# Optimization experiments

Measured on AMD Instinct MI355X. Metric: run time of the kernel, lower is better.

## Reference

```python
import jax, jax.numpy as jnp
import numpy as np

DECAY = 0.999
EPS = 1e-5
COMMIT = 0.25
ORTHO_W = 10.0
NUM_ORTHO = 128


def setup_inputs() -> dict:
    key = jax.random.key(0)
    k1, k2 = jax.random.split(key)
    M, D = 2048, 512
    B, T = 32, 1024
    x = jax.random.normal(k1, (B, T, D), dtype=jnp.float32)
    init_bound = 1.0 / M
    emb = jax.random.uniform(k2, (M, D), minval=-init_bound, maxval=init_bound, dtype=jnp.float32)
    return {
        "x": x,
        "embedding": emb,
        "ema_count": jnp.zeros((M,), jnp.float32),
        "ema_weight": emb,  # torch init: ema_weight = embedding.clone()
    }


def reference(x, embedding, ema_count, ema_weight):
    M, D = embedding.shape
    x_sg = jax.lax.stop_gradient(x)
    x_flat = x_sg.reshape(-1, D)  # [N, D]

    distances = (jnp.sum(embedding * embedding, axis=1)[None, :]
                 + jnp.sum(x_flat * x_flat, axis=1, keepdims=True)
                 - 2.0 * (x_flat @ embedding.T))
    indices = jnp.argmin(distances.astype(jnp.float32), axis=-1)  # [N]

    quantized = embedding[indices].reshape(x.shape)

    # EMA updates (training=True). one_hot(indices).sum(0) == scatter-add counts;
    # encodings.T @ x_flat == scatter-add of x rows into code slots.
    counts = jnp.zeros((M,), x.dtype).at[indices].add(1.0)
    new_count = DECAY * ema_count + (1.0 - DECAY) * counts
    n = jnp.sum(new_count)
    new_count = (new_count + EPS) / (n + M * EPS) * n
    dw = jnp.zeros((M, D), x.dtype).at[indices].add(x_flat)
    new_weight = DECAY * ema_weight + (1.0 - DECAY) * dw
    new_embedding = new_weight / new_count[:, None]

    codebook_loss = jnp.mean((x_sg - quantized) ** 2)
    e_latent_loss = jnp.mean((x - jax.lax.stop_gradient(quantized)) ** 2)
    commitment_loss = COMMIT * e_latent_loss

    quant_st = x + jax.lax.stop_gradient(quantized - x)  # straight-through

    # ortho loss over used codes of the UPDATED codebook (torch: self.embedding post-EMA).
    # Deterministic jit-safe variant of unique+randperm: take the first NUM_ORTHO
    # used code ids (stable argsort puts used codes first), mask padding if fewer.
    used = counts > 0
    order = jnp.argsort(jnp.where(used, 0, 1).astype(jnp.int32))  # stable sort
    sel = order[:NUM_ORTHO]
    valid = used[sel].astype(x.dtype)  # [NUM_ORTHO]
    codebk = new_embedding[sel]
    norm = jnp.maximum(jnp.linalg.norm(codebk, axis=-1, keepdims=True), 1e-12)
    normed = (codebk / norm) * valid[:, None]
    cosine_sim = normed @ normed.T
    n_valid = jnp.sum(valid)
    ortho_loss = jnp.sum((cosine_sim - jnp.diag(valid)) ** 2) / (n_valid * n_valid) * ORTHO_W

    return (quant_st, commitment_loss, codebook_loss, ortho_loss, indices,
            new_embedding, new_count, new_weight)
```

## Files before the change

### kernel.cpp

```cpp
#include <hip/hip_runtime.h>
#include <math.h>

#define N_ROWS 32768
#define M_CODES 2048
#define D_DIM 512
#define MARGIN 1.2e-3f
#define CAND_CAP 32

#define OUT_QST       0
#define OUT_COMMIT    16777216
#define OUT_CODEBOOK  16777217
#define OUT_ORTHO     16777218
#define OUT_INDICES   16777219
#define OUT_NEWEMB    16809987
#define OUT_NEWCOUNT  17858563
#define OUT_NEWW      17860611

#define WS_COUNTS     0
#define WS_CURSOR     2048
#define WS_SSE        4096
#define WS_ORTHO      4097
#define WS_CANDCNT    4104
#define WS_ZERO_FLOATS 36872
#define WS_E2         36872
#define WS_X2         38920
#define WS_IDX        71688
#define WS_NCN        104456
#define WS_SEL        106504
#define WS_VALID      106632
#define WS_NVALID     106760
#define WS_NORMED     106768
#define WS_NORMEDT    172304
#define WS_OFFS       237840
#define WS_ORDER      239896
#define WS_CANDC      272664
#define WS_CANDD      1321240
#define WS_XH         2369816
#define WS_EH         10758424
#define WS_TOTAL_FLOATS 11282712

typedef __attribute__((ext_vector_type(8))) short short8v;
typedef __attribute__((ext_vector_type(4))) float f32x4;

__device__ __forceinline__ unsigned short f2bf(float f) {
    unsigned u = __float_as_uint(f);
    unsigned r = (u + 0x7fffu + ((u >> 16) & 1u)) >> 16;
    return (unsigned short)r;
}
__device__ __forceinline__ int fkey(float f) {
    int b = __float_as_int(f);
    return b >= 0 ? b : (b ^ 0x7fffffff);
}
__device__ __forceinline__ float kinv(int k) {
    int b = k >= 0 ? k : (k ^ 0x7fffffff);
    return __int_as_float(b);
}

#define GLOAD16(g, s) __builtin_amdgcn_global_load_lds( \
    (const __attribute__((address_space(1))) void*)(g), \
    (__attribute__((address_space(3))) void*)(s), 16, 0, 0)

__global__ __launch_bounds__(256) void prep_kernel(const float* __restrict__ emb,
                                                   const float* __restrict__ x,
                                                   float* __restrict__ e2,
                                                   float* __restrict__ x2,
                                                   unsigned short* __restrict__ xh,
                                                   unsigned short* __restrict__ eh) {
    int row  = blockIdx.x * 4 + (threadIdx.x >> 6);
    int lane = threadIdx.x & 63;
    bool is_e = row < M_CODES;
    const float* src = is_e ? (emb + (size_t)row * D_DIM)
                            : (x + (size_t)(row - M_CODES) * D_DIM);
    unsigned short* dh = is_e ? (eh + (size_t)row * D_DIM)
                              : (xh + (size_t)(row - M_CODES) * D_DIM);
    float4 a = *(const float4*)(src + lane * 4);
    float4 b = *(const float4*)(src + 256 + lane * 4);
    float s = a.x*a.x + a.y*a.y + a.z*a.z + a.w*a.w
            + b.x*b.x + b.y*b.y + b.z*b.z + b.w*b.w;
#pragma unroll
    for (int o = 32; o > 0; o >>= 1) s += __shfl_xor(s, o, 64);

    ushort4 h0, h1;
    h0.x = f2bf(a.x); h0.y = f2bf(a.y); h0.z = f2bf(a.z); h0.w = f2bf(a.w);
    h1.x = f2bf(b.x); h1.y = f2bf(b.y); h1.z = f2bf(b.z); h1.w = f2bf(b.w);
    *(ushort4*)(dh + lane * 4)       = h0;
    *(ushort4*)(dh + 256 + lane * 4) = h1;

    if (lane == 0) {
        if (is_e) e2[row] = s;
        else      x2[row - M_CODES] = s;
    }
}

__global__ __launch_bounds__(256) void sq_kernel(const float* __restrict__ emb,
                                                 const float* __restrict__ x,
                                                 float* __restrict__ e2,
                                                 float* __restrict__ x2) {
    int row  = blockIdx.x * 4 + (threadIdx.x >> 6);
    int lane = threadIdx.x & 63;
    const float* src = (row < M_CODES) ? (emb + (size_t)row * D_DIM)
                                       : (x + (size_t)(row - M_CODES) * D_DIM);
    float4 a = *(const float4*)(src + lane * 4);
    float4 b = *(const float4*)(src + 256 + lane * 4);
    float s = a.x*a.x + a.y*a.y + a.z*a.z + a.w*a.w
            + b.x*b.x + b.y*b.y + b.z*b.z + b.w*b.w;
#pragma unroll
    for (int o = 32; o > 0; o >>= 1) s += __shfl_xor(s, o, 64);
    if (lane == 0) {
        if (row < M_CODES) e2[row] = s;
        else               x2[row - M_CODES] = s;
    }
}

__global__ __launch_bounds__(256) void approx_kernel(const unsigned short* __restrict__ xh,
                                                     const unsigned short* __restrict__ eh,
                                                     const float* __restrict__ e2g,
                                                     int* __restrict__ candcnt,
                                                     int* __restrict__ candC,
                                                     float* __restrict__ candD) {
    __shared__ short Ah[128 * 64], Bh[128 * 64];
    __shared__ int rowminI[128];

    const int t = threadIdx.x;
    const int w = t >> 6;
    const int l = t & 63;
    const int ml = l & 15;
    const int q  = l >> 4;
    const int rw = (w & 1) * 64;
    const int cw = (w >> 1) * 64;

    const int bid = blockIdx.x;
    const int row_tile = (bid >> 5) * 8 + (bid & 7);
    const int sub = (bid >> 3) & 3;
    const int row0 = row_tile * 128;
    const int code_base = sub * 512;

    if (t < 128) rowminI[t] = 0x7fffffff;

    const int grow = l >> 3;
    const int pg8  = (((l & 7) ^ grow)) * 8;

    for (int ct = 0; ct < 4; ++ct) {
        const int code0 = code_base + ct * 128;

        f32x4 acc[4][4];
#pragma unroll
        for (int mi = 0; mi < 4; ++mi)
#pragma unroll
            for (int ni = 0; ni < 4; ++ni) acc[mi][ni] = (f32x4)0.f;

        for (int k0 = 0; k0 < D_DIM; k0 += 64) {
            __syncthreads();
#pragma unroll
            for (int i = 0; i < 4; ++i) {
                int r = i * 32 + w * 8 + grow;
                GLOAD16(xh + (size_t)(row0 + r) * D_DIM + k0 + pg8, &Ah[i * 2048 + w * 512]);
                GLOAD16(eh + (size_t)(code0 + r) * D_DIM + k0 + pg8, &Bh[i * 2048 + w * 512]);
            }
            __syncthreads();

#pragma unroll
            for (int kk = 0; kk < 64; kk += 32) {
                const int pbase = kk >> 3;
                short8v a[4];
#pragma unroll
                for (int mi = 0; mi < 4; ++mi) {
                    int m = rw + mi * 16 + ml;
                    a[mi] = *(const short8v*)(&Ah[m * 64 + ((((pbase + q) ^ (m & 7))) << 3)]);
                }
#pragma unroll
                for (int ni = 0; ni < 4; ++ni) {
                    int n = cw + ni * 16 + ml;
                    short8v b = *(const short8v*)(&Bh[n * 64 + ((((pbase + q) ^ (n & 7))) << 3)]);
#pragma unroll
                    for (int mi = 0; mi < 4; ++mi)
                        acc[mi][ni] = __builtin_amdgcn_mfma_f32_16x16x32_bf16(a[mi], b, acc[mi][ni], 0, 0, 0);
                }
            }
        }

        float e2v[4];
#pragma unroll
        for (int ni = 0; ni < 4; ++ni) e2v[ni] = e2g[code0 + cw + ni * 16 + ml];

#pragma unroll
        for (int mi = 0; mi < 4; ++mi)
#pragma unroll
            for (int ni = 0; ni < 4; ++ni)
#pragma unroll
                for (int r = 0; r < 4; ++r)
                    acc[mi][ni][r] = e2v[ni] - 2.0f * acc[mi][ni][r];

#pragma unroll
        for (int mi = 0; mi < 4; ++mi)
#pragma unroll
            for (int r = 0; r < 4; ++r) {
                float v = fminf(fminf(acc[mi][0][r], acc[mi][1][r]),
                                fminf(acc[mi][2][r], acc[mi][3][r]));
#pragma unroll
                for (int o = 1; o < 16; o <<= 1) v = fminf(v, __shfl_xor(v, o, 64));
                if (ml == 0) atomicMin(&rowminI[rw + mi * 16 + q * 4 + r], fkey(v));
            }
        __syncthreads();

#pragma unroll
        for (int mi = 0; mi < 4; ++mi)
#pragma unroll
            for (int r = 0; r < 4; ++r) {
                int row_l = rw + mi * 16 + q * 4 + r;
                float rm = kinv(rowminI[row_l]);
                int row_g = row0 + row_l;
#pragma unroll
                for (int ni = 0; ni < 4; ++ni) {
                    float d = acc[mi][ni][r];
                    if (d <= rm + MARGIN) {
                        int pos = atomicAdd(&candcnt[row_g], 1);
                        if (pos < CAND_CAP) {
                            candC[row_g * CAND_CAP + pos] = code0 + cw + ni * 16 + ml;
                            candD[row_g * CAND_CAP + pos] = d;
                        }
                    }
                }
            }
    }
}

__global__ __launch_bounds__(256) void rerank_kernel(const float* __restrict__ x,
                                                     const float* __restrict__ emb,
                                                     const float* __restrict__ e2,
                                                     const float* __restrict__ x2,
                                                     const int* __restrict__ candcnt,
                                                     const int* __restrict__ candC,
                                                     const float* __restrict__ candD,
                                                     float* __restrict__ counts,
                                                     int* __restrict__ idx_out,
                                                     float* __restrict__ idxf_out) {
    const int w = threadIdx.x >> 6;
    const int lane = threadIdx.x & 63;
    const int row = blockIdx.x * 4 + w;

    int cnt = candcnt[row];
    int best_c;

    if (cnt > CAND_CAP) {
        const float x2r = x2[row];
        const float* xr = x + (size_t)row * D_DIM;
        float bd = 3.0e38f;
        int   bc = 0x7fffffff;
        for (int c = lane; c < M_CODES; c += 64) {
            const float* er = emb + (size_t)c * D_DIM;
            float dot = 0.f;
            for (int k = 0; k < D_DIM; ++k) dot = fmaf(xr[k], er[k], dot);
            float d = (x2r + e2[c]) - 2.0f * dot;
            if (d < bd || (d == bd && c < bc)) { bd = d; bc = c; }
        }
#pragma unroll
        for (int o = 32; o > 0; o >>= 1) {
            float od = __shfl_xor(bd, o, 64);
            int   oc = __shfl_xor(bc, o, 64);
            if (od < bd || (od == bd && oc < bc)) { bd = od; bc = oc; }
        }
        best_c = bc;
    } else {
        float d = 3.0e38f;
        int   c = 0x7fffffff;
        if (lane < cnt) {
            d = candD[row * CAND_CAP + lane];
            c = candC[row * CAND_CAP + lane];
        }
        float dmin = d;
#pragma unroll
        for (int o = 32; o > 0; o >>= 1) dmin = fminf(dmin, __shfl_xor(dmin, o, 64));

        bool surv = (lane < cnt) && (d <= dmin + MARGIN);
        unsigned long long mask = __ballot(surv);

        if (__popcll(mask) == 1) {
            int src = __ffsll((long long)mask) - 1;
            best_c = __shfl(c, src, 64);
        } else {
            const float x2r = x2[row];
            const float* xr = x + (size_t)row * D_DIM;
            float4 xa = *(const float4*)(xr + lane * 8);
            float4 xb = *(const float4*)(xr + lane * 8 + 4);
            float bd = 3.0e38f;
            int   bc = 0x7fffffff;
            unsigned long long m = mask;
            while (m) {
                int src = __ffsll((long long)m) - 1;
                m &= m - 1;
                int cs = __shfl(c, src, 64);
                const float* er = emb + (size_t)cs * D_DIM;
                float4 ea = *(const float4*)(er + lane * 8);
                float4 eb = *(const float4*)(er + lane * 8 + 4);
                float dot = xa.x*ea.x + xa.y*ea.y + xa.z*ea.z + xa.w*ea.w
                          + xb.x*eb.x + xb.y*eb.y + xb.z*eb.z + xb.w*eb.w;
#pragma unroll
                for (int o = 32; o > 0; o >>= 1) dot += __shfl_xor(dot, o, 64);
                float t1 = x2r + e2[cs];
                float dex = t1 - 2.0f * dot;
                if (dex < bd || (dex == bd && cs < bc)) { bd = dex; bc = cs; }
            }
            best_c = bc;
        }
    }
    if (lane == 0) {
        idx_out[row] = best_c;
        idxf_out[row] = (float)best_c;
        atomicAdd(&counts[best_c], 1.0f);
    }
}

__global__ __launch_bounds__(256) void argmin_kernel(const float* __restrict__ x,
                                                     const float* __restrict__ emb,
                                                     const float* __restrict__ e2,
                                                     const float* __restrict__ x2,
                                                     int* __restrict__ idx_out,
                                                     float* __restrict__ idxf_out) {
    __shared__ float As[64][36];
    __shared__ float Bs[32][68];
    __shared__ float e2s[64];
    __shared__ float redD[64][17];
    __shared__ int   redI[64][17];

    const int t  = threadIdx.x;
    const int tx = t & 15;
    const int ty = t >> 4;
    const int row0 = blockIdx.x * 64;

    float rmin[4];
    int   ridx[4];
#pragma unroll
    for (int r = 0; r < 4; ++r) { rmin[r] = 3.0e38f; ridx[r] = 0; }

    float x2r[4];
#pragma unroll
    for (int r = 0; r < 4; ++r) x2r[r] = x2[row0 + ty * 4 + r];

    const int lr = t >> 3;
    const int lc = t & 7;

    for (int m0 = 0; m0 < M_CODES; m0 += 64) {
        __syncthreads();
        if (t < 64) e2s[t] = e2[m0 + t];

        float acc[4][4];
#pragma unroll
        for (int r = 0; r < 4; ++r)
#pragma unroll
            for (int c = 0; c < 4; ++c) acc[r][c] = 0.f;

        for (int k0 = 0; k0 < D_DIM; k0 += 32) {
            __syncthreads();
#pragma unroll
            for (int p = 0; p < 2; ++p) {
                int r = p * 32 + lr;
                float4 v = *(const float4*)(x + (size_t)(row0 + r) * D_DIM + k0 + lc * 4);
                *(float4*)(&As[r][lc * 4]) = v;
            }
#pragma unroll
            for (int p = 0; p < 2; ++p) {
                int r = p * 32 + lr;
                float4 v = *(const float4*)(emb + (size_t)(m0 + r) * D_DIM + k0 + lc * 4);
                Bs[lc * 4 + 0][r] = v.x;
                Bs[lc * 4 + 1][r] = v.y;
                Bs[lc * 4 + 2][r] = v.z;
                Bs[lc * 4 + 3][r] = v.w;
            }
            __syncthreads();

#pragma unroll
            for (int kk = 0; kk < 32; kk += 4) {
                float av[4][4], bv[4][4];
#pragma unroll
                for (int r = 0; r < 4; ++r) {
                    float4 a4 = *(const float4*)(&As[ty * 4 + r][kk]);
                    av[r][0] = a4.x; av[r][1] = a4.y; av[r][2] = a4.z; av[r][3] = a4.w;
                }
#pragma unroll
                for (int j = 0; j < 4; ++j) {
                    float4 b4 = *(const float4*)(&Bs[kk + j][tx * 4]);
                    bv[j][0] = b4.x; bv[j][1] = b4.y; bv[j][2] = b4.z; bv[j][3] = b4.w;
                }
#pragma unroll
                for (int j = 0; j < 4; ++j)
#pragma unroll
                    for (int r = 0; r < 4; ++r)
#pragma unroll
                        for (int c = 0; c < 4; ++c)
                            acc[r][c] += av[r][j] * bv[j][c];
            }
        }

#pragma unroll
        for (int c = 0; c < 4; ++c) {
            int mm = tx * 4 + c;
            int m  = m0 + mm;
            float e2v = e2s[mm];
#pragma unroll
            for (int r = 0; r < 4; ++r) {
                float t1 = x2r[r] + e2v;
                float dd  = t1 - 2.0f * acc[r][c];
                if (dd < rmin[r]) { rmin[r] = dd; ridx[r] = m; }
            }
        }
    }

    __syncthreads();
#pragma unroll
    for (int r = 0; r < 4; ++r) {
        redD[ty * 4 + r][tx] = rmin[r];
        redI[ty * 4 + r][tx] = ridx[r];
    }
    __syncthreads();
    if (t < 64) {
        float best = redD[t][0];
        int   bi   = redI[t][0];
#pragma unroll
        for (int i = 1; i < 16; ++i) {
            float dd = redD[t][i];
            int   ii = redI[t][i];
            if (dd < best || (dd == best && ii < bi)) { best = dd; bi = ii; }
        }
        idx_out[row0 + t]  = bi;
        idxf_out[row0 + t] = (float)bi;
    }
}

__global__ __launch_bounds__(256) void hist_kernel(const int* __restrict__ idx,
                                                   float* __restrict__ counts) {
    int r = blockIdx.x * 256 + threadIdx.x;
    atomicAdd(&counts[idx[r]], 1.0f);
}

__global__ __launch_bounds__(256) void qst_sse_kernel(const float* __restrict__ x,
                                                      const float* __restrict__ emb,
                                                      const int* __restrict__ idx,
                                                      float* __restrict__ sse,
                                                      float* __restrict__ qst) {
    const int w    = threadIdx.x >> 6;
    const int lane = threadIdx.x & 63;
    const int rowbase = blockIdx.x * 16 + w * 4;
    float loss = 0.f;
    for (int i = 0; i < 4; ++i) {
        const int row = rowbase + i;
        const int m   = idx[row];
#pragma unroll
        for (int j = 0; j < 2; ++j) {
            const int off = j * 256 + lane * 4;
            float4 xv = *(const float4*)(x + (size_t)row * D_DIM + off);
            float4 qv = *(const float4*)(emb + (size_t)m * D_DIM + off);
            float4 qs;
            qs.x = xv.x + (qv.x - xv.x);
            qs.y = xv.y + (qv.y - xv.y);
            qs.z = xv.z + (qv.z - xv.z);
            qs.w = xv.w + (qv.w - xv.w);
            *(float4*)(qst + (size_t)row * D_DIM + off) = qs;
            float dx;
            dx = xv.x - qv.x; loss += dx * dx;
            dx = xv.y - qv.y; loss += dx * dx;
            dx = xv.z - qv.z; loss += dx * dx;
            dx = xv.w - qv.w; loss += dx * dx;
        }
    }
#pragma unroll
    for (int o = 32; o > 0; o >>= 1) loss += __shfl_xor(loss, o, 64);
    if (lane == 0) atomicAdd(sse, loss);
}

__global__ __launch_bounds__(256) void f1_kernel(const float* __restrict__ ema_count,
                                                 const float* __restrict__ counts,
                                                 float* __restrict__ out_newcount,
                                                 float* __restrict__ nc_ws) {
    __shared__ float red[256];
    int t = threadIdx.x;
    float raw[8];
    float part = 0.f;
#pragma unroll
    for (int i = 0; i < 8; ++i) {
        int m = t * 8 + i;
        raw[i] = 0.999f * ema_count[m] + 0.001f * counts[m];
        part += raw[i];
    }
    red[t] = part;
    __syncthreads();
    for (int s = 128; s > 0; s >>= 1) {
        if (t < s) red[t] += red[t + s];
        __syncthreads();
    }
    float n = red[0];
    float denom = n + (float)M_CODES * 1e-5f;
#pragma unroll
    for (int i = 0; i < 8; ++i) {
        int m = t * 8 + i;
        float v = (raw[i] + 1e-5f) / denom * n;
        out_newcount[m] = v;
        nc_ws[m] = v;
    }
}

__global__ __launch_bounds__(256) void scan_kernel(const float* __restrict__ counts,
                                                   int* __restrict__ offs) {
    __shared__ int pre[257];
    int t = threadIdx.x;
    int c[8];
    int s = 0;
#pragma unroll
    for (int i = 0; i < 8; ++i) { c[i] = (int)counts[t * 8 + i]; s += c[i]; }
    pre[t] = s;
    __syncthreads();
    if (t == 0) {
        int run = 0;
        for (int i = 0; i < 256; ++i) { int v = pre[i]; pre[i] = run; run += v; }
        pre[256] = run;
    }
    __syncthreads();
    int base = pre[t];
#pragma unroll
    for (int i = 0; i < 8; ++i) { offs[t * 8 + i] = base; base += c[i]; }
}

__global__ __launch_bounds__(256) void fill_kernel(const int* __restrict__ idx,
                                                   const int* __restrict__ offs,
                                                   int* __restrict__ cursor,
                                                   int* __restrict__ order) {
    int r = blockIdx.x * 256 + threadIdx.x;
    int m = idx[r];
    int pos = atomicAdd(&cursor[m], 1);
    order[offs[m] + pos] = r;
}

__global__ __launch_bounds__(256) void gather_nw_kernel(const float* __restrict__ x,
                                                        const float* __restrict__ ema_weight,
                                                        const float* __restrict__ ncn,
                                                        const float* __restrict__ counts,
                                                        const int* __restrict__ offs,
                                                        const int* __restrict__ order,
                                                        float* __restrict__ out_ne,
                                                        float* __restrict__ out_nw) {
    const int m = blockIdx.x;
    const int t = threadIdx.x;
    const int beg = offs[m];
    const int end = beg + (int)counts[m];
    float ax = 0.f, ay = 0.f;
    for (int j = beg; j < end; ++j) {
        int r = order[j];
        float2 v = *(const float2*)(x + (size_t)r * D_DIM + t * 2);
        ax += v.x; ay += v.y;
    }
    size_t i = (size_t)m * D_DIM + t * 2;
    float2 wv = *(const float2*)(ema_weight + i);
    float  c  = ncn[m];
    float2 nw, ne;
    nw.x = 0.999f * wv.x + 0.001f * ax; ne.x = nw.x / c;
    nw.y = 0.999f * wv.y + 0.001f * ay; ne.y = nw.y / c;
    *(float2*)(out_nw + i) = nw;
    *(float2*)(out_ne + i) = ne;
}

__global__ __launch_bounds__(256) void g1_kernel(const float* __restrict__ counts,
                                                 const float* __restrict__ new_emb,
                                                 int* __restrict__ sel,
                                                 float* __restrict__ valid,
                                                 float* __restrict__ n_valid,
                                                 float* __restrict__ normed,
                                                 float* __restrict__ normedT) {
    __shared__ int pre[257];
    int t = threadIdx.x;
    int u = 0;
#pragma unroll
    for (int i = 0; i < 8; ++i) u += (counts[t * 8 + i] > 0.f) ? 1 : 0;
    pre[t] = u;
    __syncthreads();
    if (t == 0) {
        int run = 0;
        for (int i = 0; i < 256; ++i) { int c = pre[i]; pre[i] = run; run += c; }
        pre[256] = run;
    }
    __syncthreads();
    int U = pre[256];
    int base = pre[t];
    int run = 0;
    for (int i = 0; i < 8; ++i) {
        int m = t * 8 + i;
        bool used = counts[m] > 0.f;
        int ur = base + run;
        if (used) {
            if (ur < 128) sel[ur] = m;
            run++;
        } else {
            int pos = U + (m - ur);
            if (pos < 128) sel[pos] = m;
        }
    }
    __syncthreads();
    if (t < 128) valid[t] = (counts[sel[t]] > 0.f) ? 1.f : 0.f;
    __syncthreads();
    if (t == 0) {
        float s = 0.f;
        for (int i = 0; i < 128; ++i) s += valid[i];
        *n_valid = s;
    }
    int w = t >> 6, lane = t & 63;
    for (int r = w; r < 128; r += 4) {
        int sm = sel[r];
        const float* src = new_emb + (size_t)sm * D_DIM;
        float4 a = *(const float4*)(src + lane * 4);
        float4 b = *(const float4*)(src + 256 + lane * 4);
        float s = a.x*a.x + a.y*a.y + a.z*a.z + a.w*a.w
                + b.x*b.x + b.y*b.y + b.z*b.z + b.w*b.w;
#pragma unroll
        for (int o = 32; o > 0; o >>= 1) s += __shfl_xor(s, o, 64);
        float norm = fmaxf(sqrtf(s), 1e-12f);
        float vv = valid[r];
        float4 na, nb;
        na.x = a.x / norm * vv; na.y = a.y / norm * vv;
        na.z = a.z / norm * vv; na.w = a.w / norm * vv;
        nb.x = b.x / norm * vv; nb.y = b.y / norm * vv;
        nb.z = b.z / norm * vv; nb.w = b.w / norm * vv;
        *(float4*)(normed + (size_t)r * D_DIM + lane * 4) = na;
        *(float4*)(normed + (size_t)r * D_DIM + 256 + lane * 4) = nb;
        normedT[(lane * 4 + 0) * 128 + r] = na.x;
        normedT[(lane * 4 + 1) * 128 + r] = na.y;
        normedT[(lane * 4 + 2) * 128 + r] = na.z;
        normedT[(lane * 4 + 3) * 128 + r] = na.w;
        normedT[(256 + lane * 4 + 0) * 128 + r] = nb.x;
        normedT[(256 + lane * 4 + 1) * 128 + r] = nb.y;
        normedT[(256 + lane * 4 + 2) * 128 + r] = nb.z;
        normedT[(256 + lane * 4 + 3) * 128 + r] = nb.w;
    }
}

__global__ __launch_bounds__(128) void g2_kernel(const float* __restrict__ normed,
                                                 const float* __restrict__ normedT,
                                                 const float* __restrict__ valid,
                                                 float* __restrict__ ortho_acc) {
    __shared__ float rowi[512];
    __shared__ float red[128];
    int i = blockIdx.x, t = threadIdx.x;
    *(float4*)(rowi + t * 4) = *(const float4*)(normed + (size_t)i * D_DIM + t * 4);
    __syncthreads();
    float dot = 0.f;
    for (int k = 0; k < D_DIM; ++k) dot += rowi[k] * normedT[k * 128 + t];
    float diag = (i == t) ? valid[i] : 0.f;
    float d = dot - diag;
    red[t] = d * d;
    __syncthreads();
    for (int s = 64; s > 0; s >>= 1) {
        if (t < s) red[t] += red[t + s];
        __syncthreads();
    }
    if (t == 0) atomicAdd(ortho_acc, red[0]);
}

__global__ void g3_kernel(const float* __restrict__ sse,
                          const float* __restrict__ ortho_acc,
                          const float* __restrict__ n_valid,
                          float* __restrict__ out3) {
    if (threadIdx.x == 0 && blockIdx.x == 0) {
        float m = *sse / 16777216.f;
        out3[0] = 0.25f * m;
        out3[1] = m;
        float nv = *n_valid;
        out3[2] = *ortho_acc / (nv * nv) * 10.f;
    }
}

extern "C" void kernel_launch(void* const* d_in, const int* in_sizes, int n_in,
                              void* d_out, int out_size, void* d_ws, size_t ws_size,
                              hipStream_t stream) {
    const float* x          = (const float*)d_in[0];
    const float* emb        = (const float*)d_in[1];
    const float* ema_count  = (const float*)d_in[2];
    const float* ema_weight = (const float*)d_in[3];
    float* out = (float*)d_out;
    float* ws  = (float*)d_ws;

    float* counts  = ws + WS_COUNTS;
    int*   cursor  = (int*)(ws + WS_CURSOR);
    float* sse     = ws + WS_SSE;
    float* ortho   = ws + WS_ORTHO;
    int*   candcnt = (int*)(ws + WS_CANDCNT);
    float* e2      = ws + WS_E2;
    float* x2      = ws + WS_X2;
    int*   idxws   = (int*)(ws + WS_IDX);
    float* ncn     = ws + WS_NCN;
    int*   sel     = (int*)(ws + WS_SEL);
    float* valid   = ws + WS_VALID;
    float* nvalid  = ws + WS_NVALID;
    float* normed  = ws + WS_NORMED;
    float* normedT = ws + WS_NORMEDT;
    int*   offs    = (int*)(ws + WS_OFFS);
    int*   order   = (int*)(ws + WS_ORDER);
    int*   candC   = (int*)(ws + WS_CANDC);
    float* candD   = ws + WS_CANDD;
    unsigned short* xh = (unsigned short*)(ws + WS_XH);
    unsigned short* eh = (unsigned short*)(ws + WS_EH);

    const bool big_ws = ws_size >= (size_t)WS_TOTAL_FLOATS * sizeof(float);

    hipMemsetAsync(ws, 0, (size_t)WS_ZERO_FLOATS * sizeof(float), stream);

    if (big_ws) {
        prep_kernel<<<(M_CODES + N_ROWS) / 4, 256, 0, stream>>>(emb, x, e2, x2, xh, eh);
        approx_kernel<<<1024, 256, 0, stream>>>(xh, eh, e2, candcnt, candC, candD);
        rerank_kernel<<<N_ROWS / 4, 256, 0, stream>>>(x, emb, e2, x2, candcnt, candC, candD,
                                                      counts, idxws, out + OUT_INDICES);
    } else {
        sq_kernel<<<(M_CODES + N_ROWS) / 4, 256, 0, stream>>>(emb, x, e2, x2);
        argmin_kernel<<<N_ROWS / 64, 256, 0, stream>>>(x, emb, e2, x2, idxws,
                                                       out + OUT_INDICES);
        hist_kernel<<<N_ROWS / 256, 256, 0, stream>>>(idxws, counts);
    }

    qst_sse_kernel<<<N_ROWS / 16, 256, 0, stream>>>(x, emb, idxws, sse, out + OUT_QST);

    f1_kernel<<<1, 256, 0, stream>>>(ema_count, counts, out + OUT_NEWCOUNT, ncn);

    scan_kernel<<<1, 256, 0, stream>>>(counts, offs);

    fill_kernel<<<N_ROWS / 256, 256, 0, stream>>>(idxws, offs, cursor, order);

    gather_nw_kernel<<<M_CODES, 256, 0, stream>>>(x, ema_weight, ncn, counts, offs, order,
                                                  out + OUT_NEWEMB, out + OUT_NEWW);

    g1_kernel<<<1, 256, 0, stream>>>(counts, out + OUT_NEWEMB, sel, valid, nvalid,
                                     normed, normedT);

    g2_kernel<<<128, 128, 0, stream>>>(normed, normedT, valid, ortho);

    g3_kernel<<<1, 64, 0, stream>>>(sse, ortho, nvalid, out + OUT_COMMIT);
}
```

Measured before the change: 559.3 us.

## Rewrite approximate distance GEMM with register-resident X fragments and direct global B loads

Replaces the LDS-tiled bf16 MFMA approximate-distance kernel with one where each wave keeps its 32 rows of X for the full 512-wide K in registers and streams codebook fragments straight from global memory (relying on cache) in 64-code chunks. Each block now covers 1024 codes instead of 512, and the running row minimum is held in registers per wave instead of a shared atomicMin, so the LDS staging and block-wide syncs go away. Because the candidate threshold now uses a running minimum, more candidates may be emitted early in the scan, which raises atomic traffic and the risk of overflowing the candidate cap. Holding 32 short8 vectors of X per lane also adds heavy register pressure.

```diff
diff --git a/kernel.cpp b/kernel.cpp
--- a/kernel.cpp
+++ b/kernel.cpp
@@ -47,18 +47,6 @@
     unsigned r = (u + 0x7fffu + ((u >> 16) & 1u)) >> 16;
     return (unsigned short)r;
 }
-__device__ __forceinline__ int fkey(float f) {
-    int b = __float_as_int(f);
-    return b >= 0 ? b : (b ^ 0x7fffffff);
-}
-__device__ __forceinline__ float kinv(int k) {
-    int b = k >= 0 ? k : (k ^ 0x7fffffff);
-    return __int_as_float(b);
-}
-
-#define GLOAD16(g, s) __builtin_amdgcn_global_load_lds( \
-    (const __attribute__((address_space(1))) void*)(g), \
-    (__attribute__((address_space(3))) void*)(s), 16, 0, 0)
 
 __global__ __launch_bounds__(256) void prep_kernel(const float* __restrict__ emb,
                                                    const float* __restrict__ x,
@@ -112,112 +100,95 @@
     }
 }
 
-__global__ __launch_bounds__(256) void approx_kernel(const unsigned short* __restrict__ xh,
-                                                     const unsigned short* __restrict__ eh,
-                                                     const float* __restrict__ e2g,
-                                                     int* __restrict__ candcnt,
-                                                     int* __restrict__ candC,
-                                                     float* __restrict__ candD) {
-    __shared__ short Ah[128 * 64], Bh[128 * 64];
-    __shared__ int rowminI[128];
-
-    const int t = threadIdx.x;
-    const int w = t >> 6;
-    const int l = t & 63;
+__global__ __launch_bounds__(256) void approx2_kernel(const unsigned short* __restrict__ xh,
+                                                      const unsigned short* __restrict__ eh,
+                                                      const float* __restrict__ e2g,
+                                                      int* __restrict__ candcnt,
+                                                      int* __restrict__ candC,
+                                                      float* __restrict__ candD) {
+    const int t  = threadIdx.x;
+    const int w  = t >> 6;
+    const int l  = t & 63;
     const int ml = l & 15;
     const int q  = l >> 4;
-    const int rw = (w & 1) * 64;
-    const int cw = (w >> 1) * 64;
-
-    const int bid = blockIdx.x;
-    const int row_tile = (bid >> 5) * 8 + (bid & 7);
-    const int sub = (bid >> 3) & 3;
-    const int row0 = row_tile * 128;
-    const int code_base = sub * 512;
-
-    if (t < 128) rowminI[t] = 0x7fffffff;
-
-    const int grow = l >> 3;
-    const int pg8  = (((l & 7) ^ grow)) * 8;
-
-    for (int ct = 0; ct < 4; ++ct) {
-        const int code0 = code_base + ct * 128;
-
-        f32x4 acc[4][4];
-#pragma unroll
-        for (int mi = 0; mi < 4; ++mi)
+
+    const int row0      = (blockIdx.x >> 1) * 128 + w * 32;
+    const int code_base = (blockIdx.x & 1) * 1024;
+
+    short8v af[2][16];
+#pragma unroll
+    for (int mi = 0; mi < 2; ++mi) {
+        const unsigned short* ar = xh + (size_t)(row0 + mi * 16 + ml) * D_DIM + q * 8;
+#pragma unroll
+        for (int kk = 0; kk < 16; ++kk)
+            af[mi][kk] = *(const short8v*)(ar + kk * 32);
+    }
+
+    float rmin[2][4];
+#pragma unroll
+    for (int mi = 0; mi < 2; ++mi)
+#pragma unroll
+        for (int r = 0; r < 4; ++r) rmin[mi][r] = 3.0e38f;
+
+    for (int ch = 0; ch < 16; ++ch) {
+        __builtin_amdgcn_s_barrier();
+
+        const int code0 = code_base + ch * 64;
+
+        f32x4 acc[2][4];
+#pragma unroll
+        for (int mi = 0; mi < 2; ++mi)
 #pragma unroll
             for (int ni = 0; ni < 4; ++ni) acc[mi][ni] = (f32x4)0.f;
 
-        for (int k0 = 0; k0 < D_DIM; k0 += 64) {
-            __syncthreads();
-#pragma unroll
-            for (int i = 0; i < 4; ++i) {
-                int r = i * 32 + w * 8 + grow;
-                GLOAD16(xh + (size_t)(row0 + r) * D_DIM + k0 + pg8, &Ah[i * 2048 + w * 512]);
-                GLOAD16(eh + (size_t)(code0 + r) * D_DIM + k0 + pg8, &Bh[i * 2048 + w * 512]);
+        const unsigned short* br = eh + (size_t)(code0 + ml) * D_DIM + q * 8;
+#pragma unroll
+        for (int kk = 0; kk < 16; ++kk) {
+            short8v b0 = *(const short8v*)(br + (size_t)(0 * 16) * D_DIM + kk * 32);
+            short8v b1 = *(const short8v*)(br + (size_t)(1 * 16) * D_DIM + kk * 32);
+            short8v b2 = *(const short8v*)(br + (size_t)(2 * 16) * D_DIM + kk * 32);
+            short8v b3 = *(const short8v*)(br + (size_t)(3 * 16) * D_DIM + kk * 32);
+            acc[0][0] = __builtin_amdgcn_mfma_f32_16x16x32_bf16(af[0][kk], b0, acc[0][0], 0, 0, 0);
+            acc[1][0] = __builtin_amdgcn_mfma_f32_16x16x32_bf16(af[1][kk], b0, acc[1][0], 0, 0, 0);
+            acc[0][1] = __builtin_amdgcn_mfma_f32_16x16x32_bf16(af[0][kk], b1, acc[0][1], 0, 0, 0);
+            acc[1][1] = __builtin_amdgcn_mfma_f32_16x16x32_bf16(af[1][kk], b1, acc[1][1], 0, 0, 0);
+            acc[0][2] = __builtin_amdgcn_mfma_f32_16x16x32_bf16(af[0][kk], b2, acc[0][2], 0, 0, 0);
+            acc[1][2] = __builtin_amdgcn_mfma_f32_16x16x32_bf16(af[1][kk], b2, acc[1][2], 0, 0, 0);
+            acc[0][3] = __builtin_amdgcn_mfma_f32_16x16x32_bf16(af[0][kk], b3, acc[0][3], 0, 0, 0);
+            acc[1][3] = __builtin_amdgcn_mfma_f32_16x16x32_bf16(af[1][kk], b3, acc[1][3], 0, 0, 0);
+        }
+
+        float e2v[4];
+#pragma unroll
+        for (int ni = 0; ni < 4; ++ni) e2v[ni] = e2g[code0 + ni * 16 + ml];
+
+#pragma unroll
+        for (int mi = 0; mi < 2; ++mi)
+#pragma unroll
+            for (int r = 0; r < 4; ++r) {
+                float v = fminf(fminf(e2v[0] - 2.0f * acc[mi][0][r],
+                                      e2v[1] - 2.0f * acc[mi][1][r]),
+                                fminf(e2v[2] - 2.0f * acc[mi][2][r],
+                                      e2v[3] - 2.0f * acc[mi][3][r]));
+#pragma unroll
+                for (int o = 1; o < 16; o <<= 1) v = fminf(v, __shfl_xor(v, o, 64));
+                rmin[mi][r] = fminf(rmin[mi][r], v);
             }
-            __syncthreads();
-
-#pragma unroll
-            for (int kk = 0; kk < 64; kk += 32) {
-                const int pbase = kk >> 3;
-                short8v a[4];
-#pragma unroll
-                for (int mi = 0; mi < 4; ++mi) {
-                    int m = rw + mi * 16 + ml;
-                    a[mi] = *(const short8v*)(&Ah[m * 64 + ((((pbase + q) ^ (m & 7))) << 3)]);
-                }
+
+#pragma unroll
+        for (int mi = 0; mi < 2; ++mi)
+#pragma unroll
+            for (int r = 0; r < 4; ++r) {
+                const float rm = rmin[mi][r] + MARGIN;
+                const int row_g = row0 + mi * 16 + q * 4 + r;
 #pragma unroll
                 for (int ni = 0; ni < 4; ++ni) {
-                    int n = cw + ni * 16 + ml;
-                    short8v b = *(const short8v*)(&Bh[n * 64 + ((((pbase + q) ^ (n & 7))) << 3)]);
-#pragma unroll
-                    for (int mi = 0; mi < 4; ++mi)
-                        acc[mi][ni] = __builtin_amdgcn_mfma_f32_16x16x32_bf16(a[mi], b, acc[mi][ni], 0, 0, 0);
-                }
-            }
-        }
-
-        float e2v[4];
-#pragma unroll
-        for (int ni = 0; ni < 4; ++ni) e2v[ni] = e2g[code0 + cw + ni * 16 + ml];
-
-#pragma unroll
-        for (int mi = 0; mi < 4; ++mi)
-#pragma unroll
-            for (int ni = 0; ni < 4; ++ni)
-#pragma unroll
-                for (int r = 0; r < 4; ++r)
-                    acc[mi][ni][r] = e2v[ni] - 2.0f * acc[mi][ni][r];
-
-#pragma unroll
-        for (int mi = 0; mi < 4; ++mi)
-#pragma unroll
-            for (int r = 0; r < 4; ++r) {
-                float v = fminf(fminf(acc[mi][0][r], acc[mi][1][r]),
-                                fminf(acc[mi][2][r], acc[mi][3][r]));
-#pragma unroll
-                for (int o = 1; o < 16; o <<= 1) v = fminf(v, __shfl_xor(v, o, 64));
-                if (ml == 0) atomicMin(&rowminI[rw + mi * 16 + q * 4 + r], fkey(v));
-            }
-        __syncthreads();
-
-#pragma unroll
-        for (int mi = 0; mi < 4; ++mi)
-#pragma unroll
-            for (int r = 0; r < 4; ++r) {
-                int row_l = rw + mi * 16 + q * 4 + r;
-                float rm = kinv(rowminI[row_l]);
-                int row_g = row0 + row_l;
-#pragma unroll
-                for (int ni = 0; ni < 4; ++ni) {
-                    float d = acc[mi][ni][r];
-                    if (d <= rm + MARGIN) {
+                    float dd = e2v[ni] - 2.0f * acc[mi][ni][r];
+                    if (dd <= rm) {
                         int pos = atomicAdd(&candcnt[row_g], 1);
                         if (pos < CAND_CAP) {
-                            candC[row_g * CAND_CAP + pos] = code0 + cw + ni * 16 + ml;
-                            candD[row_g * CAND_CAP + pos] = d;
+                            candC[row_g * CAND_CAP + pos] = code0 + ni * 16 + ml;
+                            candD[row_g * CAND_CAP + pos] = dd;
                         }
                     }
                 }
@@ -703,7 +674,7 @@
 
     if (big_ws) {
         prep_kernel<<<(M_CODES + N_ROWS) / 4, 256, 0, stream>>>(emb, x, e2, x2, xh, eh);
-        approx_kernel<<<1024, 256, 0, stream>>>(xh, eh, e2, candcnt, candC, candD);
+        approx2_kernel<<<512, 256, 0, stream>>>(xh, eh, e2, candcnt, candC, candD);
         rerank_kernel<<<N_ROWS / 4, 256, 0, stream>>>(x, emb, e2, x2, candcnt, candC, candD,
                                                       counts, idxws, out + OUT_INDICES);
     } else {
```

Measured after the change: 688.2 us. +23.1%, slower.
